# Optimization experiments

Hardware: AMD Instinct MI355X
Metric: run time of the kernel (lower is better)

Reference implementation:

```python
import jax, jax.numpy as jnp
import numpy as np

N = 50000   # total nodes
G = 500     # number of graphs
E = 800000  # edges
K = 5       # Chebyshev order


def cheb_conv(x, edge_index, W, b):
    """PyG ChebConv with sym normalization, lambda_max=2.0.
    L_hat = (2/lambda_max)(I - D^-1/2 A D^-1/2) - I = -D^-1/2 A D^-1/2.
    out = sum_k T_k(L_hat) x @ W[k] + b, with Chebyshev recurrence.
    W: [K, in, out].
    """
    row, col = edge_index[0], edge_index[1]
    deg = jax.ops.segment_sum(jnp.ones_like(row, dtype=x.dtype), row, num_segments=N)
    dinv = jnp.where(deg > 0, jax.lax.rsqrt(jnp.maximum(deg, 1e-12)), 0.0).astype(x.dtype)
    norm = -dinv[row] * dinv[col]  # [E]

    def Lx(h):  # sparse matvec: gather -> scale -> scatter-add
        return jax.ops.segment_sum(norm[:, None] * h[col], row, num_segments=N)

    Tx0 = x
    out = Tx0 @ W[0]
    Tx1 = Lx(Tx0)
    out = out + Tx1 @ W[1]
    for k in range(2, W.shape[0]):
        Tx2 = 2.0 * Lx(Tx1) - Tx0
        out = out + Tx2 @ W[k]
        Tx0, Tx1 = Tx1, Tx2
    return out + b


def setup_inputs() -> dict:
    key = jax.random.key(0)
    ks = jax.random.split(key, 12)
    F_in, C = 116, 2
    dims = [(F_in, 32), (32, 32), (32, 64), (64, 64), (64, 128)]
    inp = {}
    inp["x"] = jax.random.normal(ks[0], (N, F_in), dtype=jnp.float32)
    inp["edge_index"] = jax.random.randint(ks[1], (2, E), 0, N, dtype=jnp.int32)
    inp["batch"] = jnp.sort(jax.random.randint(ks[2], (N,), 0, G, dtype=jnp.int32))
    for i, (di, do) in enumerate(dims):
        scale = 1.0 / np.sqrt(di * K)
        inp[f"W{i+1}"] = jax.random.normal(ks[3 + i], (K, di, do), dtype=jnp.float32) * scale
        inp[f"b{i+1}"] = jnp.zeros((do,), dtype=jnp.float32)
    inp["lin_w"] = jax.random.normal(ks[10], (128, C), dtype=jnp.float32) * (1.0 / np.sqrt(128))
    inp["lin_b"] = jnp.zeros((C,), dtype=jnp.float32)
    return inp


def reference(x, edge_index, batch, W1, b1, W2, b2, W3, b3, W4, b4, W5, b5, lin_w, lin_b):
    h = jax.nn.relu(cheb_conv(x, edge_index, W1, b1))
    h = jax.nn.relu(cheb_conv(h, edge_index, W2, b2))
    # dropout is identity in eval mode
    h = jax.nn.relu(cheb_conv(h, edge_index, W3, b3))
    h = jax.nn.relu(cheb_conv(h, edge_index, W4, b4))
    h = jax.nn.relu(cheb_conv(h, edge_index, W5, b5))
    # global mean pool over graph ids
    cnt = jax.ops.segment_sum(jnp.ones((N,), h.dtype), batch, num_segments=G)
    summ = jax.ops.segment_sum(h, batch, num_segments=G)  # [G, 128]
    pooled = summ / jnp.maximum(cnt, 1.0)[:, None]
    logits = pooled @ lin_w + lin_b  # [G, C]
    return jax.nn.log_softmax(logits, axis=1)
```

## Files before the change

kernel.cpp:

```cpp
#include <hip/hip_runtime.h>

#define N_NODES 50000
#define N_GRAPHS 500
#define N_EDGES 800000

static inline int cdiv(int a, int b) { return (a + b - 1) / b; }

typedef _Float16 half8v __attribute__((ext_vector_type(8)));
typedef _Float16 half4v __attribute__((ext_vector_type(4)));
typedef __attribute__((ext_vector_type(4))) float f32x4;

__device__ __forceinline__ _Float16 f2h(float f) { return (_Float16)f; }


__global__ void count_kernel(const int* __restrict__ row, int* __restrict__ cnt, int e) {
    int t = blockIdx.x * blockDim.x + threadIdx.x;
    if (t < e) atomicAdd(&cnt[row[t]], 1);
}

__global__ void block_scan_kernel(const int* __restrict__ cnt, int* __restrict__ rp,
                                  int* __restrict__ bsum, int n) {
    __shared__ int buf[2][256];
    int t = threadIdx.x;
    int idx = blockIdx.x * 256 + t;
    int v = (idx < n) ? cnt[idx] : 0;
    buf[0][t] = v;
    __syncthreads();
    int s = 0;
#pragma unroll
    for (int off = 1; off < 256; off <<= 1) {
        int x = buf[s][t];
        if (t >= off) x += buf[s][t - off];
        buf[s ^ 1][t] = x;
        s ^= 1;
        __syncthreads();
    }
    if (idx < n) rp[idx] = buf[s][t] - v;
    if (t == 255) bsum[blockIdx.x] = buf[s][255];
}

__global__ void scan_bsum_kernel(int* __restrict__ bsum, int nb) {
    __shared__ int buf[2][256];
    int t = threadIdx.x;
    int v = (t < nb) ? bsum[t] : 0;
    buf[0][t] = v;
    __syncthreads();
    int s = 0;
#pragma unroll
    for (int off = 1; off < 256; off <<= 1) {
        int x = buf[s][t];
        if (t >= off) x += buf[s][t - off];
        buf[s ^ 1][t] = x;
        s ^= 1;
        __syncthreads();
    }
    if (t < nb) bsum[t] = buf[s][t] - v;
}

__global__ void add_off_kernel(int* __restrict__ rp, const int* __restrict__ bsum, int n) {
    int idx = blockIdx.x * 256 + threadIdx.x;
    if (idx < n) rp[idx] += bsum[idx >> 8];
    if (idx == 0) rp[n] = N_EDGES;
}

__global__ void dinv_cursor_kernel(const int* __restrict__ cnt, const int* __restrict__ rp,
                                   float* __restrict__ dinv, int* __restrict__ cursor, int n) {
    int t = blockIdx.x * blockDim.x + threadIdx.x;
    if (t < n) {
        int c = cnt[t];
        dinv[t] = (c > 0) ? rsqrtf((float)c) : 0.0f;
        cursor[t] = rp[t];
    }
}

__global__ void fill_kernel(const int* __restrict__ row, const int* __restrict__ col,
                            const float* __restrict__ dinv, int* __restrict__ cursor,
                            unsigned* __restrict__ ew, int e) {
    int t = blockIdx.x * blockDim.x + threadIdx.x;
    if (t < e) {
        int r = row[t], c = col[t];
        int slot = atomicAdd(&cursor[r], 1);
        float w = -dinv[r] * dinv[c];
        unsigned short wb = __builtin_bit_cast(unsigned short, (_Float16)w);
        ew[slot] = ((unsigned)c << 16) | (unsigned)wb;
    }
}


__global__ void conv_x_kernel(const float* __restrict__ x, _Float16* __restrict__ xh) {
    int t = blockIdx.x * blockDim.x + threadIdx.x;
    if (t >= N_NODES * 128) return;
    int r = t >> 7, c = t & 127;
    xh[t] = (c < 116) ? f2h(x[(size_t)r * 116 + c]) : (_Float16)0.f;
}

__global__ void conv_wt1_kernel(const float* __restrict__ W, _Float16* __restrict__ wt) {
    int t = blockIdx.x * blockDim.x + threadIdx.x;
    if (t >= 160 * 128) return;
    int c = t >> 7, k = t & 127;
    wt[t] = (k < 116) ? f2h(W[(c >> 5) * (116 * 32) + k * 32 + (c & 31)]) : (_Float16)0.f;
}

template <int FOUT, int KB>
__global__ void conv_wt_kernel(const float* __restrict__ W, _Float16* __restrict__ wt) {
    int t = blockIdx.x * blockDim.x + threadIdx.x;
    if (t >= FOUT * KB) return;
    int c = t / KB, k = t % KB;
    wt[t] = f2h(W[(size_t)k * FOUT + c]);
}


template <int F, bool HAS_A, bool HAS_B, bool RELU>
__global__ __launch_bounds__(256) void spmm_fused(
    const int* __restrict__ rp, const unsigned* __restrict__ ew,
    const _Float16* __restrict__ src, int ld_s, float alpha,
    const _Float16* __restrict__ A, int ldA, float cA,
    const _Float16* __restrict__ B, int ldB, float cB,
    const float* __restrict__ bias, _Float16* __restrict__ outh, int ldO) {
    constexpr int TPN = F / 4;
    int t = blockIdx.x * blockDim.x + threadIdx.x;
    if (t >= N_NODES * TPN) return;
    int node = t / TPN;
    int f = (t % TPN) * 4;
    const _Float16* sf = src + f;
    int e0 = rp[node], e1 = rp[node + 1];
    float ax = 0.f, ay = 0.f, az = 0.f, aw = 0.f;
    int j = e0;
    for (; j + 7 < e1; j += 8) {
        unsigned e_[8];
#pragma unroll
        for (int u = 0; u < 8; ++u) e_[u] = ew[j + u];
        half4v v_[8];
#pragma unroll
        for (int u = 0; u < 8; ++u) v_[u] = *(const half4v*)(sf + (size_t)(e_[u] >> 16) * ld_s);
#pragma unroll
        for (int u = 0; u < 8; ++u) {
            float w = (float)__builtin_bit_cast(_Float16, (unsigned short)e_[u]);
            ax += w * (float)v_[u].x;
            ay += w * (float)v_[u].y;
            az += w * (float)v_[u].z;
            aw += w * (float)v_[u].w;
        }
    }
    for (; j + 3 < e1; j += 4) {
        unsigned e_[4];
#pragma unroll
        for (int u = 0; u < 4; ++u) e_[u] = ew[j + u];
        half4v v_[4];
#pragma unroll
        for (int u = 0; u < 4; ++u) v_[u] = *(const half4v*)(sf + (size_t)(e_[u] >> 16) * ld_s);
#pragma unroll
        for (int u = 0; u < 4; ++u) {
            float w = (float)__builtin_bit_cast(_Float16, (unsigned short)e_[u]);
            ax += w * (float)v_[u].x;
            ay += w * (float)v_[u].y;
            az += w * (float)v_[u].z;
            aw += w * (float)v_[u].w;
        }
    }
    for (; j < e1; ++j) {
        unsigned ea = ew[j];
        float w0 = (float)__builtin_bit_cast(_Float16, (unsigned short)ea);
        half4v v0 = *(const half4v*)(sf + (size_t)(ea >> 16) * ld_s);
        ax += w0 * (float)v0.x;
        ay += w0 * (float)v0.y;
        az += w0 * (float)v0.z;
        aw += w0 * (float)v0.w;
    }
    float rx = alpha * ax, ry = alpha * ay, rz = alpha * az, rw = alpha * aw;
    if (HAS_A) {
        half4v a4 = *(const half4v*)(A + (size_t)node * ldA + f);
        rx += cA * (float)a4.x; ry += cA * (float)a4.y;
        rz += cA * (float)a4.z; rw += cA * (float)a4.w;
    }
    if (HAS_B) {
        half4v b4 = *(const half4v*)(B + (size_t)node * ldB + f);
        rx += cB * (float)b4.x; ry += cB * (float)b4.y;
        rz += cB * (float)b4.z; rw += cB * (float)b4.w;
    }
    if (RELU) {
        float4 bb = *(const float4*)(bias + f);
        rx = fmaxf(rx + bb.x, 0.f); ry = fmaxf(ry + bb.y, 0.f);
        rz = fmaxf(rz + bb.z, 0.f); rw = fmaxf(rw + bb.w, 0.f);
    }
    half4v h4;
    h4.x = f2h(rx); h4.y = f2h(ry); h4.z = f2h(rz); h4.w = f2h(rw);
    *(half4v*)(outh + (size_t)node * ldO + f) = h4;
}


template <int KB, int F0, int FOUT, bool DUAL, bool RELU>
__global__ __launch_bounds__(256) void mm_mfma(const _Float16* __restrict__ A0h,
                                               const _Float16* __restrict__ A1h,
                                               const _Float16* __restrict__ Wt,
                                               const float* __restrict__ bias,
                                               _Float16* __restrict__ outh) {
    constexpr int NT = FOUT / 16;
    constexpr int LD1 = (KB - F0) > 0 ? (KB - F0) : 1;
    constexpr int KC = (KB > 160) ? 160 : KB;
    constexpr int NCH = KB / KC;
    constexpr int LDW = KC + 8;
    __shared__ _Float16 lw[FOUT][LDW];

    int tid = threadIdx.x;
    int l = tid & 63;
    int w = tid >> 6;
    int row0 = blockIdx.x * 64 + w * 16;
    int r15 = l & 15;
    int kg = l >> 4;
    int rr = row0 + r15;
    if (rr > N_NODES - 1) rr = N_NODES - 1;

    f32x4 acc[NT];
#pragma unroll
    for (int ct = 0; ct < NT; ++ct) acc[ct] = (f32x4){0.f, 0.f, 0.f, 0.f};

#pragma unroll
    for (int ch = 0; ch < NCH; ++ch) {
        constexpr int C8 = KC / 8;
        int c0 = ch * KC;
        for (int idx = tid; idx < FOUT * C8; idx += 256) {
            int r = idx / C8, c8 = idx - r * C8;
            *(half8v*)&lw[r][c8 * 8] = *(const half8v*)(Wt + (size_t)r * KB + c0 + c8 * 8);
        }
        __syncthreads();
#pragma unroll
        for (int k0 = 0; k0 < KC; k0 += 32) {
            int gc = c0 + k0;
            int kl = gc + kg * 8;
            const _Float16* ap;
            if (!DUAL || gc < F0)
                ap = A0h + (size_t)rr * F0 + kl;
            else
                ap = A1h + (size_t)rr * LD1 + (kl - F0);
            half8v af = *(const half8v*)ap;
#pragma unroll
            for (int ct = 0; ct < NT; ++ct) {
                half8v bf = *(const half8v*)&lw[ct * 16 + r15][k0 + kg * 8];
                acc[ct] = __builtin_amdgcn_mfma_f32_16x16x32_f16(af, bf, acc[ct], 0, 0, 0);
            }
        }
        __syncthreads();
    }

    int orow = row0 + kg * 4;
#pragma unroll
    for (int ct = 0; ct < NT; ++ct) {
        int col = ct * 16 + r15;
        float bv = RELU ? bias[col] : 0.f;
#pragma unroll
        for (int i = 0; i < 4; ++i) {
            int rw = orow + i;
            if (rw < N_NODES) {
                float v = acc[ct][i];
                if (RELU) v = fmaxf(v + bv, 0.f);
                outh[(size_t)rw * FOUT + col] = f2h(v);
            }
        }
    }
}


__global__ void pool_head_kernel(const _Float16* __restrict__ h, const int* __restrict__ batch,
                                 const float* __restrict__ lw, const float* __restrict__ lb,
                                 float* __restrict__ out) {
    int g = blockIdx.x;
    int f = threadIdx.x;
    int s, e;
    {
        int lo = 0, hi = N_NODES;
        while (lo < hi) { int mid = (lo + hi) >> 1; if (batch[mid] < g) lo = mid + 1; else hi = mid; }
        s = lo;
        hi = N_NODES;
        while (lo < hi) { int mid = (lo + hi) >> 1; if (batch[mid] < g + 1) lo = mid + 1; else hi = mid; }
        e = lo;
    }
    float sum = 0.0f;
    for (int i = s; i < e; ++i) sum += (float)h[(size_t)i * 128 + f];
    float cnt = (float)(e - s);
    float pooled = sum / fmaxf(cnt, 1.0f);

    __shared__ float l0[128], l1[128];
    l0[f] = pooled * lw[f * 2 + 0];
    l1[f] = pooled * lw[f * 2 + 1];
    __syncthreads();
    for (int sdt = 64; sdt > 0; sdt >>= 1) {
        if (f < sdt) { l0[f] += l0[f + sdt]; l1[f] += l1[f + sdt]; }
        __syncthreads();
    }
    if (f == 0) {
        float a = l0[0] + lb[0], b = l1[0] + lb[1];
        float m = fmaxf(a, b);
        float lse = m + logf(expf(a - m) + expf(b - m));
        out[g * 2 + 0] = a - lse;
        out[g * 2 + 1] = b - lse;
    }
}


template <int F, int FOUT>
static void run_layer_fwd(const _Float16* hh, _Float16* Zh, _Float16* houth,
                          const _Float16* Wt, const float* b, const int* rp,
                          const unsigned* ew, hipStream_t s) {
    constexpr int TPN = F / 4;
    int sp_grid = cdiv(N_NODES * TPN, 256);
    int mm_grid = cdiv(N_NODES, 64);
    const _Float16* nh_ = nullptr;
    spmm_fused<F, false, false, false><<<sp_grid, 256, 0, s>>>(
        rp, ew, hh, F, 1.f, nh_, 0, 0.f, nh_, 0, 0.f, nullptr, Zh + 0 * F, 4 * F);
    spmm_fused<F, true, false, false><<<sp_grid, 256, 0, s>>>(
        rp, ew, Zh + 0 * F, 4 * F, 2.f, hh, F, -1.f, nh_, 0, 0.f, nullptr, Zh + 1 * F, 4 * F);
    spmm_fused<F, true, false, false><<<sp_grid, 256, 0, s>>>(
        rp, ew, Zh + 1 * F, 4 * F, 2.f, Zh + 0 * F, 4 * F, -1.f, nh_, 0, 0.f, nullptr, Zh + 2 * F, 4 * F);
    spmm_fused<F, true, false, false><<<sp_grid, 256, 0, s>>>(
        rp, ew, Zh + 2 * F, 4 * F, 2.f, Zh + 1 * F, 4 * F, -1.f, nh_, 0, 0.f, nullptr, Zh + 3 * F, 4 * F);
    mm_mfma<5 * F, F, FOUT, true, true><<<mm_grid, 256, 0, s>>>(hh, Zh, Wt, b, houth);
}

extern "C" void kernel_launch(void* const* d_in, const int* in_sizes, int n_in,
                              void* d_out, int out_size, void* d_ws, size_t ws_size,
                              hipStream_t stream) {
    const float* x = (const float*)d_in[0];
    const int* ei = (const int*)d_in[1];
    const int* batch = (const int*)d_in[2];
    const float* W1 = (const float*)d_in[3];
    const float* b1 = (const float*)d_in[4];
    const float* W2 = (const float*)d_in[5];
    const float* b2 = (const float*)d_in[6];
    const float* W3 = (const float*)d_in[7];
    const float* b3 = (const float*)d_in[8];
    const float* W4 = (const float*)d_in[9];
    const float* b4 = (const float*)d_in[10];
    const float* W5 = (const float*)d_in[11];
    const float* b5 = (const float*)d_in[12];
    const float* lin_w = (const float*)d_in[13];
    const float* lin_b = (const float*)d_in[14];
    const int* row = ei;
    const int* col = ei + N_EDGES;
    float* out = (float*)d_out;

    char* p = (char*)d_ws;
    auto alloc = [&](size_t bytes) {
        char* r = p;
        p += (bytes + 255) & ~(size_t)255;
        return r;
    };
    int* cnt = (int*)alloc((size_t)N_NODES * 4);
    int* rp = (int*)alloc((size_t)(N_NODES + 1) * 4);
    int* cursor = (int*)alloc((size_t)N_NODES * 4);
    int* bsum = (int*)alloc(256 * 4);
    float* dinv = (float*)alloc((size_t)N_NODES * 4);
    unsigned* ew = (unsigned*)alloc((size_t)N_EDGES * 4);
    _Float16* Zh = (_Float16*)alloc((size_t)N_NODES * 256 * 2);
    _Float16* hAh = (_Float16*)alloc((size_t)N_NODES * 128 * 2);
    _Float16* hBh = (_Float16*)alloc((size_t)N_NODES * 128 * 2);
    _Float16* wt1 = (_Float16*)alloc((size_t)160 * 128 * 2);
    _Float16* wt2 = (_Float16*)alloc((size_t)32 * 160 * 2);
    _Float16* wt3 = (_Float16*)alloc((size_t)64 * 160 * 2);
    _Float16* wt4 = (_Float16*)alloc((size_t)64 * 320 * 2);
    _Float16* wt5 = (_Float16*)alloc((size_t)128 * 320 * 2);

    const int NB = cdiv(N_NODES, 256);
    hipMemsetAsync(cnt, 0, (size_t)N_NODES * 4, stream);
    count_kernel<<<cdiv(N_EDGES, 256), 256, 0, stream>>>(row, cnt, N_EDGES);
    block_scan_kernel<<<NB, 256, 0, stream>>>(cnt, rp, bsum, N_NODES);
    scan_bsum_kernel<<<1, 256, 0, stream>>>(bsum, NB);
    add_off_kernel<<<NB, 256, 0, stream>>>(rp, bsum, N_NODES);
    dinv_cursor_kernel<<<cdiv(N_NODES, 256), 256, 0, stream>>>(cnt, rp, dinv, cursor, N_NODES);
    fill_kernel<<<cdiv(N_EDGES, 256), 256, 0, stream>>>(row, col, dinv, cursor, ew, N_EDGES);

    conv_x_kernel<<<cdiv(N_NODES * 128, 256), 256, 0, stream>>>(x, hAh);
    conv_wt1_kernel<<<cdiv(160 * 128, 256), 256, 0, stream>>>(W1, wt1);
    conv_wt_kernel<32, 160><<<cdiv(32 * 160, 256), 256, 0, stream>>>(W2, wt2);
    conv_wt_kernel<64, 160><<<cdiv(64 * 160, 256), 256, 0, stream>>>(W3, wt3);
    conv_wt_kernel<64, 320><<<cdiv(64 * 320, 256), 256, 0, stream>>>(W4, wt4);
    conv_wt_kernel<128, 320><<<cdiv(128 * 320, 256), 256, 0, stream>>>(W5, wt5);

    _Float16* Uh = Zh;
    const _Float16* nh_ = nullptr;
    mm_mfma<128, 128, 160, false, false><<<cdiv(N_NODES, 64), 256, 0, stream>>>(
        hAh, nh_, wt1, nullptr, Uh);
    _Float16* B3h = hBh;
    _Float16* B2h = hBh + (size_t)N_NODES * 32;
    _Float16* B1h = hBh + (size_t)N_NODES * 64;
    _Float16* h1h = hAh;
    int g32 = cdiv(N_NODES * 8, 256);
    spmm_fused<32, true, false, false><<<g32, 256, 0, stream>>>(
        rp, ew, Uh + 128, 160, 2.f, Uh + 96, 160, 1.f, nh_, 0, 0.f, nullptr, B3h, 32);
    spmm_fused<32, true, true, false><<<g32, 256, 0, stream>>>(
        rp, ew, B3h, 32, 2.f, Uh + 64, 160, 1.f, Uh + 128, 160, -1.f, nullptr, B2h, 32);
    spmm_fused<32, true, true, false><<<g32, 256, 0, stream>>>(
        rp, ew, B2h, 32, 2.f, Uh + 32, 160, 1.f, B3h, 32, -1.f, nullptr, B1h, 32);
    spmm_fused<32, true, true, true><<<g32, 256, 0, stream>>>(
        rp, ew, B1h, 32, 1.f, Uh + 0, 160, 1.f, B2h, 32, -1.f, b1, h1h, 32);

    run_layer_fwd<32, 32>(h1h, Zh, hBh, wt2, b2, rp, ew, stream);
    run_layer_fwd<32, 64>(hBh, Zh, hAh, wt3, b3, rp, ew, stream);
    run_layer_fwd<64, 64>(hAh, Zh, hBh, wt4, b4, rp, ew, stream);
    run_layer_fwd<64, 128>(hBh, Zh, hAh, wt5, b5, rp, ew, stream);

    pool_head_kernel<<<N_GRAPHS, 128, 0, stream>>>(hAh, batch, lin_w, lin_b, out);
}
```

Baseline: 621.0 us.

## Two-pass bucketed CSR fill and merge conversion kernels into one launch

Replaces the direct scatter fill of the CSR edge array with a two-pass scheme. The first pass bins edges into 128-node row buckets using shared-memory histograms and one global atomic per bucket per block, writing to a staging buffer. The second pass places each staged edge into its final slot, so the scattered writes and per-row atomics hit a local region instead of the whole array. It also fuses the six input and weight conversion kernels into a single launch, at the cost of an extra 6.4MB staging buffer and an extra pass over the edges.

```diff
diff --git a/kernel.cpp b/kernel.cpp
--- a/kernel.cpp
+++ b/kernel.cpp
@@ -3,6 +3,9 @@
 #define N_NODES 50000
 #define N_GRAPHS 500
 #define N_EDGES 800000
+#define BUCK_SHIFT 7
+#define NBUCK 391
+#define EPB_A 8192
 
 static inline int cdiv(int a, int b) { return (a + b - 1) / b; }
 
@@ -64,49 +67,91 @@
 }
 
 __global__ void dinv_cursor_kernel(const int* __restrict__ cnt, const int* __restrict__ rp,
-                                   float* __restrict__ dinv, int* __restrict__ cursor, int n) {
+                                   float* __restrict__ dinv, int* __restrict__ cursor,
+                                   int* __restrict__ gcur, int n) {
     int t = blockIdx.x * blockDim.x + threadIdx.x;
     if (t < n) {
         int c = cnt[t];
         dinv[t] = (c > 0) ? rsqrtf((float)c) : 0.0f;
         cursor[t] = rp[t];
     }
-}
-
-__global__ void fill_kernel(const int* __restrict__ row, const int* __restrict__ col,
-                            const float* __restrict__ dinv, int* __restrict__ cursor,
-                            unsigned* __restrict__ ew, int e) {
+    if (t < NBUCK) gcur[t] = rp[t << BUCK_SHIFT];
+}
+
+__global__ __launch_bounds__(256) void bin_kernel(
+    const int* __restrict__ row, const int* __restrict__ col,
+    const float* __restrict__ dinv, int* __restrict__ gcur,
+    int2* __restrict__ stage, int e) {
+    __shared__ int lhist[NBUCK];
+    __shared__ int lbase[NBUCK];
+    int tid = threadIdx.x;
+    int base = blockIdx.x * EPB_A;
+    for (int b = tid; b < NBUCK; b += 256) lhist[b] = 0;
+    __syncthreads();
+#pragma unroll
+    for (int u = 0; u < EPB_A / 256; ++u) {
+        int e_ = base + u * 256 + tid;
+        if (e_ < e) atomicAdd(&lhist[row[e_] >> BUCK_SHIFT], 1);
+    }
+    __syncthreads();
+    for (int b = tid; b < NBUCK; b += 256) {
+        int c = lhist[b];
+        lbase[b] = c ? atomicAdd(&gcur[b], c) : 0;
+        lhist[b] = 0;
+    }
+    __syncthreads();
+#pragma unroll
+    for (int u = 0; u < EPB_A / 256; ++u) {
+        int e_ = base + u * 256 + tid;
+        if (e_ < e) {
+            int r = row[e_], c = col[e_];
+            int b = r >> BUCK_SHIFT;
+            int pos = lbase[b] + atomicAdd(&lhist[b], 1);
+            float w = -dinv[r] * dinv[c];
+            unsigned short wb = __builtin_bit_cast(unsigned short, (_Float16)w);
+            stage[pos] = make_int2(r, (int)(((unsigned)c << 16) | (unsigned)wb));
+        }
+    }
+}
+
+__global__ void place_kernel(const int2* __restrict__ stage, int* __restrict__ cursor,
+                             unsigned* __restrict__ ew, int e) {
     int t = blockIdx.x * blockDim.x + threadIdx.x;
     if (t < e) {
-        int r = row[t], c = col[t];
-        int slot = atomicAdd(&cursor[r], 1);
-        float w = -dinv[r] * dinv[c];
-        unsigned short wb = __builtin_bit_cast(unsigned short, (_Float16)w);
-        ew[slot] = ((unsigned)c << 16) | (unsigned)wb;
-    }
-}
-
-
-__global__ void conv_x_kernel(const float* __restrict__ x, _Float16* __restrict__ xh) {
+        int2 s = stage[t];
+        int pos = atomicAdd(&cursor[s.x], 1);
+        ew[pos] = (unsigned)s.y;
+    }
+}
+
+
+__global__ void conv_all_kernel(const float* __restrict__ x, const float* __restrict__ W1,
+                                const float* __restrict__ W2, const float* __restrict__ W3,
+                                const float* __restrict__ W4, const float* __restrict__ W5,
+                                _Float16* __restrict__ xh, _Float16* __restrict__ wt1,
+                                _Float16* __restrict__ wt2, _Float16* __restrict__ wt3,
+                                _Float16* __restrict__ wt4, _Float16* __restrict__ wt5) {
     int t = blockIdx.x * blockDim.x + threadIdx.x;
-    if (t >= N_NODES * 128) return;
-    int r = t >> 7, c = t & 127;
-    xh[t] = (c < 116) ? f2h(x[(size_t)r * 116 + c]) : (_Float16)0.f;
-}
-
-__global__ void conv_wt1_kernel(const float* __restrict__ W, _Float16* __restrict__ wt) {
-    int t = blockIdx.x * blockDim.x + threadIdx.x;
-    if (t >= 160 * 128) return;
-    int c = t >> 7, k = t & 127;
-    wt[t] = (k < 116) ? f2h(W[(c >> 5) * (116 * 32) + k * 32 + (c & 31)]) : (_Float16)0.f;
-}
-
-template <int FOUT, int KB>
-__global__ void conv_wt_kernel(const float* __restrict__ W, _Float16* __restrict__ wt) {
-    int t = blockIdx.x * blockDim.x + threadIdx.x;
-    if (t >= FOUT * KB) return;
-    int c = t / KB, k = t % KB;
-    wt[t] = f2h(W[(size_t)k * FOUT + c]);
+    const int NX = N_NODES * 128;
+    if (t < NX) {
+        int r = t >> 7, c = t & 127;
+        xh[t] = (c < 116) ? f2h(x[(size_t)r * 116 + c]) : (_Float16)0.f;
+        return;
+    }
+    t -= NX;
+    if (t < 160 * 128) {
+        int c = t >> 7, k = t & 127;
+        wt1[t] = (k < 116) ? f2h(W1[(c >> 5) * (116 * 32) + k * 32 + (c & 31)]) : (_Float16)0.f;
+        return;
+    }
+    t -= 160 * 128;
+    if (t < 32 * 160) { int c = t / 160, k = t % 160; wt2[t] = f2h(W2[(size_t)k * 32 + c]); return; }
+    t -= 32 * 160;
+    if (t < 64 * 160) { int c = t / 160, k = t % 160; wt3[t] = f2h(W3[(size_t)k * 64 + c]); return; }
+    t -= 64 * 160;
+    if (t < 64 * 320) { int c = t / 320, k = t % 320; wt4[t] = f2h(W4[(size_t)k * 64 + c]); return; }
+    t -= 64 * 320;
+    if (t < 128 * 320) { int c = t / 320, k = t % 320; wt5[t] = f2h(W5[(size_t)k * 128 + c]); }
 }
 
 
@@ -349,8 +394,10 @@
     int* rp = (int*)alloc((size_t)(N_NODES + 1) * 4);
     int* cursor = (int*)alloc((size_t)N_NODES * 4);
     int* bsum = (int*)alloc(256 * 4);
+    int* gcur = (int*)alloc((size_t)NBUCK * 4);
     float* dinv = (float*)alloc((size_t)N_NODES * 4);
     unsigned* ew = (unsigned*)alloc((size_t)N_EDGES * 4);
+    int2* stage = (int2*)alloc((size_t)N_EDGES * 8);
     _Float16* Zh = (_Float16*)alloc((size_t)N_NODES * 256 * 2);
     _Float16* hAh = (_Float16*)alloc((size_t)N_NODES * 128 * 2);
     _Float16* hBh = (_Float16*)alloc((size_t)N_NODES * 128 * 2);
@@ -366,15 +413,14 @@
     block_scan_kernel<<<NB, 256, 0, stream>>>(cnt, rp, bsum, N_NODES);
     scan_bsum_kernel<<<1, 256, 0, stream>>>(bsum, NB);
     add_off_kernel<<<NB, 256, 0, stream>>>(rp, bsum, N_NODES);
-    dinv_cursor_kernel<<<cdiv(N_NODES, 256), 256, 0, stream>>>(cnt, rp, dinv, cursor, N_NODES);
-    fill_kernel<<<cdiv(N_EDGES, 256), 256, 0, stream>>>(row, col, dinv, cursor, ew, N_EDGES);
-
-    conv_x_kernel<<<cdiv(N_NODES * 128, 256), 256, 0, stream>>>(x, hAh);
-    conv_wt1_kernel<<<cdiv(160 * 128, 256), 256, 0, stream>>>(W1, wt1);
-    conv_wt_kernel<32, 160><<<cdiv(32 * 160, 256), 256, 0, stream>>>(W2, wt2);
-    conv_wt_kernel<64, 160><<<cdiv(64 * 160, 256), 256, 0, stream>>>(W3, wt3);
-    conv_wt_kernel<64, 320><<<cdiv(64 * 320, 256), 256, 0, stream>>>(W4, wt4);
-    conv_wt_kernel<128, 320><<<cdiv(128 * 320, 256), 256, 0, stream>>>(W5, wt5);
+    dinv_cursor_kernel<<<cdiv(N_NODES, 256), 256, 0, stream>>>(cnt, rp, dinv, cursor, gcur,
+                                                               N_NODES);
+    bin_kernel<<<cdiv(N_EDGES, EPB_A), 256, 0, stream>>>(row, col, dinv, gcur, stage, N_EDGES);
+    place_kernel<<<cdiv(N_EDGES, 256), 256, 0, stream>>>(stage, cursor, ew, N_EDGES);
+
+    const int CONV_TOT = N_NODES * 128 + 160 * 128 + 32 * 160 + 64 * 160 + 64 * 320 + 128 * 320;
+    conv_all_kernel<<<cdiv(CONV_TOT, 256), 256, 0, stream>>>(x, W1, W2, W3, W4, W5, hAh, wt1,
+                                                             wt2, wt3, wt4, wt5);
 
     _Float16* Uh = Zh;
     const _Float16* nh_ = nullptr;
```

After: 622.1 us. Within noise of the previous version (+0.2%).
